# Kernel tuning notes

Hardware: AMD Instinct MI355X
Metric: run time of the kernel (lower is better)

## Reference

```python
import jax, jax.numpy as jnp
import numpy as np

B, L, A, HD, H = 4096, 512, 64, 1024, 32
EPS = 1e-5


def _ln(x, g, b):
    m = jnp.mean(x, axis=-1, keepdims=True)
    v = jnp.mean((x - m) ** 2, axis=-1, keepdims=True)
    return (x - m) * jax.lax.rsqrt(v + EPS) * g + b


def setup_inputs() -> dict:
    key = jax.random.key(0)
    ks = jax.random.split(key, 12)
    s = 0.02
    return {
        "z_0": jax.random.normal(ks[0], (B, L), jnp.float32),
        "actions": jax.random.normal(ks[1], (B, H, A), jnp.float32),
        "W1": jax.random.normal(ks[2], (L + A, HD), jnp.float32) * s,
        "b1": jnp.zeros((HD,), jnp.float32),
        "g1": jnp.ones((HD,), jnp.float32),
        "be1": jnp.zeros((HD,), jnp.float32),
        "W2": jax.random.normal(ks[3], (HD, HD), jnp.float32) * s,
        "b2": jnp.zeros((HD,), jnp.float32),
        "g2": jnp.ones((HD,), jnp.float32),
        "be2": jnp.zeros((HD,), jnp.float32),
        "W3": jax.random.normal(ks[4], (HD, L), jnp.float32) * s,
        "b3": jnp.zeros((L,), jnp.float32),
        "uW1": jax.random.normal(ks[5], (L, HD // 2), jnp.float32) * s,
        "ub1": jnp.zeros((HD // 2,), jnp.float32),
        "uW2": jax.random.normal(ks[6], (HD // 2, 1), jnp.float32) * s,
        "ub2": jnp.zeros((1,), jnp.float32),
        "gate": jnp.asarray(0.5, jnp.float32),
    }


def reference(z_0, actions, W1, b1, g1, be1, W2, b2, g2, be2, W3, b3,
              uW1, ub1, uW2, ub2, gate):
    gate_s = jax.nn.sigmoid(gate)

    def step_fn(z, a):
        za = jnp.concatenate([z, a], axis=-1)              # [B, L+A]
        h = jax.nn.gelu(_ln(za @ W1 + b1, g1, be1), approximate=False)
        h = jax.nn.gelu(_ln(h @ W2 + b2, g2, be2), approximate=False)
        dz = h @ W3 + b3                                   # [B, L]
        z_next = z + gate_s * dz
        u = jax.nn.gelu(z_next @ uW1 + ub1, approximate=False)
        sigma = jax.nn.softplus(u @ uW2 + ub2)             # [B, 1]
        return z_next, (z_next, sigma)

    a_seq = jnp.swapaxes(actions, 0, 1)                    # [H, B, A]
    _, (traj, sigs) = jax.lax.scan(step_fn, z_0, a_seq)
    return jnp.swapaxes(traj, 0, 1), jnp.swapaxes(sigs, 0, 1)
```

## Files before the change

kernel.cpp:

```cpp
#include <hip/hip_runtime.h>
#include <hip/hip_bf16.h>
#include <math.h>

#define B_SZ 4096
#define L_SZ 512
#define A_SZ 64
#define HD_SZ 1024
#define H_SZ 32

typedef __attribute__((ext_vector_type(8))) short bf16x8;
typedef __attribute__((ext_vector_type(4))) short s16x4;
typedef __attribute__((ext_vector_type(4))) float f32x4;

#define GLDS16(gsrc, ldst) __builtin_amdgcn_global_load_lds(              \
    (const __attribute__((address_space(1))) void*)(gsrc),                \
    (__attribute__((address_space(3))) void*)(ldst), 16, 0, 0)

template <int N> __device__ __forceinline__ void vmwait() {
  asm volatile("s_waitcnt vmcnt(%0)" :: "n"(N) : "memory");
}

__device__ __forceinline__ float gelu_exact(float x) {
  return 0.5f * x * (1.0f + erff(x * 0.70710678118654752f));
}

template <int BM, int BN, int MODE>
__global__ __launch_bounds__(256, 2) void gemm_kernel(
    const __hip_bfloat16* __restrict__ A0, int a0s,
    const __hip_bfloat16* __restrict__ A1, int a1s, int ksplit,
    const __hip_bfloat16* __restrict__ Bt,
    const float* __restrict__ bias,
    int N, int K,
    float* __restrict__ outf,
    float* __restrict__ z_cur,
    __hip_bfloat16* __restrict__ znb,
    float* __restrict__ traj,
    const float* __restrict__ gate,
    int t,
    float* __restrict__ zu,
    const float* __restrict__ ub1v,
    const float* __restrict__ uW2,
    float* __restrict__ sig_acc,
    __hip_bfloat16* __restrict__ outb) {
  constexpr int BK = 64;
  constexpr int ROWB = BK * 2;
  constexpr int FM = BM / 32, FN = BN / 32;
  constexpr int ABYTES = BM * ROWB;
  constexpr int BUFB = (BM + BN) * ROWB;
  constexpr int LOADS = (BM + BN) / 32;
  __shared__ __align__(16) char lds[3 * BUFB];

  const int tid = threadIdx.x;
  const int m0 = blockIdx.x * BM, n0 = blockIdx.y * BN;
  const int wave = tid >> 6, lane = tid & 63;
  const int l15 = lane & 15, lg = lane >> 4;
  const int wm = wave >> 1, wn = wave & 1;
  const int NK = K / BK;

  f32x4 acc[FM][FN];
#pragma unroll
  for (int mi = 0; mi < FM; ++mi)
#pragma unroll
    for (int ni = 0; ni < FN; ++ni) acc[mi][ni] = (f32x4){0.f, 0.f, 0.f, 0.f};

  auto stage = [&](int slot, int kt) {
    char* dst = lds + slot * BUFB;
    const int k0 = kt * BK;
    const __hip_bfloat16* Aptr;
    int As, kloc;
    if (k0 < ksplit) { Aptr = A0; As = a0s; kloc = k0; }
    else             { Aptr = A1; As = a1s; kloc = k0 - ksplit; }
#pragma unroll
    for (int i = 0; i < BM / 32; ++i) {
      int off = tid * 16 + i * 4096;
      int r = off >> 7;
      int csw = (off & 127) ^ ((r & 7) << 4);
      GLDS16(Aptr + (size_t)(m0 + r) * As + kloc + (csw >> 1), dst + off);
    }
#pragma unroll
    for (int i = 0; i < BN / 32; ++i) {
      int off = tid * 16 + i * 4096;
      int r = off >> 7;
      int csw = (off & 127) ^ ((r & 7) << 4);
      GLDS16(Bt + (size_t)(n0 + r) * K + k0 + (csw >> 1), dst + ABYTES + off);
    }
  };

  const int xrow = (l15 & 7) << 4;
  const int offs0 = (lg * 16) ^ xrow;
  const int aoff = (wm * (FM * 16) + l15) * ROWB;
  const int boff = ABYTES + (wn * (FN * 16) + l15) * ROWB;

  stage(0, 0);
  stage(1, 1);

  int buf = 0;
  for (int kt = 0; kt < NK; ++kt) {
    if (kt + 2 < NK) {
      int s2 = buf + 2; if (s2 >= 3) s2 -= 3;
      stage(s2, kt + 2);
      vmwait<2 * LOADS>();
    } else if (kt + 1 < NK) {
      vmwait<LOADS>();
    } else {
      vmwait<0>();
    }
    __builtin_amdgcn_s_barrier();
    asm volatile("" ::: "memory");

    const char* lb = lds + buf * BUFB;
    bf16x8 a_[FM][2], b_[FN][2];
#pragma unroll
    for (int mi = 0; mi < FM; ++mi) {
      a_[mi][0] = *(const bf16x8*)(lb + aoff + mi * (16 * ROWB) + offs0);
      a_[mi][1] = *(const bf16x8*)(lb + aoff + mi * (16 * ROWB) + (offs0 ^ 64));
    }
#pragma unroll
    for (int ni = 0; ni < FN; ++ni) {
      b_[ni][0] = *(const bf16x8*)(lb + boff + ni * (16 * ROWB) + offs0);
      b_[ni][1] = *(const bf16x8*)(lb + boff + ni * (16 * ROWB) + (offs0 ^ 64));
    }
#pragma unroll
    for (int s = 0; s < 2; ++s)
#pragma unroll
      for (int mi = 0; mi < FM; ++mi)
#pragma unroll
        for (int ni = 0; ni < FN; ++ni)
          acc[mi][ni] = __builtin_amdgcn_mfma_f32_16x16x32_bf16(
              a_[mi][s], b_[ni][s], acc[mi][ni], 0, 0, 0);

    asm volatile("" ::: "memory");
    __builtin_amdgcn_s_barrier();
    buf = (buf + 1 == 3) ? 0 : buf + 1;
  }

  if constexpr (MODE == 0 || MODE == 5) {
#pragma unroll
    for (int mi = 0; mi < FM; ++mi) {
#pragma unroll
      for (int ni = 0; ni < FN; ++ni) {
        int gcol = n0 + wn * (FN * 16) + ni * 16 + l15;
        float bv = bias[gcol];
#pragma unroll
        for (int r = 0; r < 4; ++r) {
          int grow = m0 + wm * (FM * 16) + mi * 16 + lg * 4 + r;
          float v = acc[mi][ni][r] + bv;
          if constexpr (MODE == 0)
            outb[(size_t)grow * N + gcol] = __float2bfloat16(v);
          else
            outf[(size_t)grow * N + gcol] = v;
        }
      }
    }
  } else {
    const float gs = 1.f / (1.f + expf(-gate[0]));
    if (n0 < L_SZ) {
#pragma unroll
      for (int mi = 0; mi < FM; ++mi) {
#pragma unroll
        for (int ni = 0; ni < FN; ++ni) {
          int gcol = n0 + wn * (FN * 16) + ni * 16 + l15;
          float bv = bias[gcol];
#pragma unroll
          for (int r = 0; r < 4; ++r) {
            int grow = m0 + wm * (FM * 16) + mi * 16 + lg * 4 + r;
            size_t zi = (size_t)grow * L_SZ + gcol;
            float zn = z_cur[zi] + gs * (acc[mi][ni][r] + bv);
            z_cur[zi] = zn;
            znb[zi] = __float2bfloat16(zn);
            traj[(size_t)grow * (H_SZ * L_SZ) + (size_t)t * L_SZ + gcol] = zn;
          }
        }
      }
    } else {
#pragma unroll
      for (int mi = 0; mi < FM; ++mi) {
        float p[4] = {0.f, 0.f, 0.f, 0.f};
#pragma unroll
        for (int ni = 0; ni < FN; ++ni) {
          int gcol = n0 + wn * (FN * 16) + ni * 16 + l15;
          int j = gcol - L_SZ;
          float bv = bias[gcol];
          float ub = ub1v[j];
          float w2 = uW2[j];
#pragma unroll
          for (int r = 0; r < 4; ++r) {
            int grow = m0 + wm * (FM * 16) + mi * 16 + lg * 4 + r;
            size_t ui = (size_t)grow * L_SZ + j;
            float zun = zu[ui] + gs * (acc[mi][ni][r] + bv);
            zu[ui] = zun;
            p[r] += gelu_exact(zun + ub) * w2;
          }
        }
#pragma unroll
        for (int o = 1; o < 16; o <<= 1) {
#pragma unroll
          for (int r = 0; r < 4; ++r) p[r] += __shfl_xor(p[r], o);
        }
        if (l15 == 0) {
          int rowb = m0 + wm * (FM * 16) + mi * 16 + lg * 4;
#pragma unroll
          for (int r = 0; r < 4; ++r)
            atomicAdd(&sig_acc[(size_t)(rowb + r) * H_SZ + t], p[r]);
        }
      }
    }
  }
}

__global__ __launch_bounds__(256) void ln_gelu_kernel(
    const __hip_bfloat16* __restrict__ x, const float* __restrict__ gam,
    const float* __restrict__ bet, __hip_bfloat16* __restrict__ out) {
  constexpr int N = HD_SZ;
  const int row = blockIdx.x;
  const int tid = threadIdx.x, lane = tid & 63, wave = tid >> 6;
  union { s16x4 sv; __hip_bfloat16 h[4]; } in;
  in.sv = *(const s16x4*)(x + (size_t)row * N + tid * 4);
  float v[4];
#pragma unroll
  for (int j = 0; j < 4; ++j) v[j] = __bfloat162float(in.h[j]);
  float s = v[0] + v[1] + v[2] + v[3];
  float s2 = v[0] * v[0] + v[1] * v[1] + v[2] * v[2] + v[3] * v[3];
#pragma unroll
  for (int o = 32; o; o >>= 1) {
    s += __shfl_xor(s, o);
    s2 += __shfl_xor(s2, o);
  }
  __shared__ float as_[4], as2_[4];
  if (lane == 0) { as_[wave] = s; as2_[wave] = s2; }
  __syncthreads();
  s = as_[0] + as_[1] + as_[2] + as_[3];
  s2 = as2_[0] + as2_[1] + as2_[2] + as2_[3];
  float mean = s * (1.f / N);
  float var = s2 * (1.f / N) - mean * mean;
  float rstd = rsqrtf(var + 1e-5f);
  f32x4 g = *(const f32x4*)(gam + tid * 4);
  f32x4 b = *(const f32x4*)(bet + tid * 4);
  union { __hip_bfloat16 h[4]; s16x4 sv; } o;
#pragma unroll
  for (int j = 0; j < 4; ++j) {
    float y = (v[j] - mean) * rstd * g[j] + b[j];
    o.h[j] = __float2bfloat16(gelu_exact(y));
  }
  *(s16x4*)(out + (size_t)row * N + tid * 4) = o.sv;
}

__global__ void transpose_cvt(const float* __restrict__ in,
                              __hip_bfloat16* __restrict__ out, int K, int N) {
  __shared__ float tile[32][33];
  const int n0 = blockIdx.x * 32, k0 = blockIdx.y * 32;
  const int tx = threadIdx.x, ty = threadIdx.y;
#pragma unroll
  for (int i = 0; i < 32; i += 8)
    tile[ty + i][tx] = in[(size_t)(k0 + ty + i) * N + (n0 + tx)];
  __syncthreads();
#pragma unroll
  for (int i = 0; i < 32; i += 8)
    out[(size_t)(n0 + ty + i) * K + (k0 + tx)] = __float2bfloat16(tile[tx][ty + i]);
}

__global__ __launch_bounds__(256) void w34_kernel(
    const float* __restrict__ W3, const float* __restrict__ uW1,
    __hip_bfloat16* __restrict__ W3c) {
  __shared__ float tA[16][17];
  __shared__ float tB[16][17];
  const int k0 = blockIdx.x * 16, j0 = blockIdx.y * 16;
  const int tx = threadIdx.x & 15, ty = threadIdx.x >> 4;
  float acc = 0.f;
  for (int i0 = 0; i0 < L_SZ; i0 += 16) {
    tA[ty][tx] = W3[(size_t)(k0 + ty) * L_SZ + i0 + tx];
    tB[ty][tx] = uW1[(size_t)(i0 + ty) * (HD_SZ / 2) + j0 + tx];
    __syncthreads();
#pragma unroll
    for (int i = 0; i < 16; ++i) acc += tA[ty][i] * tB[i][tx];
    __syncthreads();
  }
  W3c[(size_t)(L_SZ + j0 + tx) * HD_SZ + k0 + ty] = __float2bfloat16(acc);
}

__global__ void bias3_kernel(const float* __restrict__ b3,
                             const float* __restrict__ uW1,
                             float* __restrict__ bias3c) {
  int j = blockIdx.x * 256 + threadIdx.x;
  if (j >= L_SZ) return;
  bias3c[j] = b3[j];
  float s = 0.f;
  for (int i = 0; i < L_SZ; ++i) s += b3[i] * uW1[(size_t)i * (HD_SZ / 2) + j];
  bias3c[L_SZ + j] = s;
}

__global__ void cvt_bf16_kernel(const float* __restrict__ in,
                                __hip_bfloat16* __restrict__ out, int n4) {
  int i = blockIdx.x * 256 + threadIdx.x;
  if (i >= n4) return;
  f32x4 v = ((const f32x4*)in)[i];
  union { __hip_bfloat16 h[4]; s16x4 sv; } o;
#pragma unroll
  for (int j = 0; j < 4; ++j) o.h[j] = __float2bfloat16(v[j]);
  ((s16x4*)out)[i] = o.sv;
}

__global__ void init_z_kernel(const float* __restrict__ z0,
                              float* __restrict__ z_cur,
                              __hip_bfloat16* __restrict__ znb, int n4) {
  int i = blockIdx.x * 256 + threadIdx.x;
  if (i >= n4) return;
  f32x4 v = ((const f32x4*)z0)[i];
  ((f32x4*)z_cur)[i] = v;
  union { __hip_bfloat16 h[4]; s16x4 sv; } o;
#pragma unroll
  for (int j = 0; j < 4; ++j) o.h[j] = __float2bfloat16(v[j]);
  ((s16x4*)znb)[i] = o.sv;
}

__global__ void zero_kernel(float* __restrict__ p, int n) {
  int i = blockIdx.x * 256 + threadIdx.x;
  if (i < n) p[i] = 0.f;
}

__global__ void softplus_kernel(const float* __restrict__ acc,
                                const float* __restrict__ ub2,
                                float* __restrict__ out, int n) {
  int i = blockIdx.x * 256 + threadIdx.x;
  if (i >= n) return;
  float v = acc[i] + ub2[0];
  out[i] = v > 20.f ? v : log1pf(expf(v));
}

extern "C" void kernel_launch(void* const* d_in, const int* in_sizes, int n_in,
                              void* d_out, int out_size, void* d_ws,
                              size_t ws_size, hipStream_t stream) {
  const float* z0      = (const float*)d_in[0];
  const float* actions = (const float*)d_in[1];
  const float* W1  = (const float*)d_in[2];
  const float* b1  = (const float*)d_in[3];
  const float* g1  = (const float*)d_in[4];
  const float* be1 = (const float*)d_in[5];
  const float* W2  = (const float*)d_in[6];
  const float* b2  = (const float*)d_in[7];
  const float* g2  = (const float*)d_in[8];
  const float* be2 = (const float*)d_in[9];
  const float* W3  = (const float*)d_in[10];
  const float* b3  = (const float*)d_in[11];
  const float* uW1 = (const float*)d_in[12];
  const float* ub1 = (const float*)d_in[13];
  const float* uW2 = (const float*)d_in[14];
  const float* ub2 = (const float*)d_in[15];
  const float* gate = (const float*)d_in[16];

  char* w = (char*)d_ws;
  __hip_bfloat16* W1t = (__hip_bfloat16*)w;  w += (size_t)(L_SZ + A_SZ) * HD_SZ * 2;
  __hip_bfloat16* W2t = (__hip_bfloat16*)w;  w += (size_t)HD_SZ * HD_SZ * 2;
  __hip_bfloat16* W3c = (__hip_bfloat16*)w;  w += (size_t)HD_SZ * HD_SZ * 2;
  __hip_bfloat16* uW1t = (__hip_bfloat16*)w; w += (size_t)L_SZ * (HD_SZ / 2) * 2;
  __hip_bfloat16* actb = (__hip_bfloat16*)w; w += (size_t)B_SZ * H_SZ * A_SZ * 2;
  float* z_cur = (float*)w;                  w += (size_t)B_SZ * L_SZ * 4;
  __hip_bfloat16* znb = (__hip_bfloat16*)w;  w += (size_t)B_SZ * L_SZ * 2;
  float* zu = (float*)w;                     w += (size_t)B_SZ * L_SZ * 4;
  __hip_bfloat16* tws = (__hip_bfloat16*)w;  w += (size_t)B_SZ * HD_SZ * 2;
  __hip_bfloat16* hb = (__hip_bfloat16*)w;   w += (size_t)B_SZ * HD_SZ * 2;
  float* sig_acc = (float*)w;                w += (size_t)B_SZ * H_SZ * 4;
  float* bias3c = (float*)w;                 w += (size_t)HD_SZ * 4;
  float* zbias = (float*)w;                  w += (size_t)L_SZ * 4;

  float* trajOut = (float*)d_out;
  float* sigsOut = (float*)d_out + (size_t)B_SZ * H_SZ * L_SZ;

  dim3 tb(32, 8);
  transpose_cvt<<<dim3(HD_SZ / 32, (L_SZ + A_SZ) / 32), tb, 0, stream>>>(W1, W1t, L_SZ + A_SZ, HD_SZ);
  transpose_cvt<<<dim3(HD_SZ / 32, HD_SZ / 32), tb, 0, stream>>>(W2, W2t, HD_SZ, HD_SZ);
  transpose_cvt<<<dim3(L_SZ / 32, HD_SZ / 32), tb, 0, stream>>>(W3, W3c, HD_SZ, L_SZ);
  transpose_cvt<<<dim3((HD_SZ / 2) / 32, L_SZ / 32), tb, 0, stream>>>(uW1, uW1t, L_SZ, HD_SZ / 2);
  w34_kernel<<<dim3(HD_SZ / 16, L_SZ / 16), 256, 0, stream>>>(W3, uW1, W3c);
  bias3_kernel<<<2, 256, 0, stream>>>(b3, uW1, bias3c);

  cvt_bf16_kernel<<<(B_SZ * H_SZ * A_SZ / 4 + 255) / 256, 256, 0, stream>>>(
      actions, actb, B_SZ * H_SZ * A_SZ / 4);
  init_z_kernel<<<(B_SZ * L_SZ / 4 + 255) / 256, 256, 0, stream>>>(
      z0, z_cur, znb, B_SZ * L_SZ / 4);
  zero_kernel<<<(B_SZ * H_SZ + 255) / 256, 256, 0, stream>>>(sig_acc, B_SZ * H_SZ);
  zero_kernel<<<(L_SZ + 255) / 256, 256, 0, stream>>>(zbias, L_SZ);

  const int KSPLIT_NONE = 1 << 30;

  gemm_kernel<64, 128, 5><<<dim3(B_SZ / 64, L_SZ / 128), 256, 0, stream>>>(
      znb, L_SZ, nullptr, 0, KSPLIT_NONE, uW1t, zbias,
      L_SZ, L_SZ, zu, nullptr, nullptr, nullptr, nullptr, 0,
      nullptr, nullptr, nullptr, nullptr, nullptr);

  for (int t = 0; t < H_SZ; ++t) {
    gemm_kernel<64, 128, 0><<<dim3(B_SZ / 64, HD_SZ / 128), 256, 0, stream>>>(
        znb, L_SZ, actb + (size_t)t * A_SZ, H_SZ * A_SZ, L_SZ, W1t, b1,
        HD_SZ, L_SZ + A_SZ, nullptr, nullptr, nullptr, nullptr, nullptr, 0,
        nullptr, nullptr, nullptr, nullptr, tws);
    ln_gelu_kernel<<<B_SZ, 256, 0, stream>>>(tws, g1, be1, hb);
    gemm_kernel<64, 128, 0><<<dim3(B_SZ / 64, HD_SZ / 128), 256, 0, stream>>>(
        hb, HD_SZ, nullptr, 0, KSPLIT_NONE, W2t, b2,
        HD_SZ, HD_SZ, nullptr, nullptr, nullptr, nullptr, nullptr, 0,
        nullptr, nullptr, nullptr, nullptr, tws);
    ln_gelu_kernel<<<B_SZ, 256, 0, stream>>>(tws, g2, be2, hb);
    gemm_kernel<64, 128, 4><<<dim3(B_SZ / 64, HD_SZ / 128), 256, 0, stream>>>(
        hb, HD_SZ, nullptr, 0, KSPLIT_NONE, W3c, bias3c,
        HD_SZ, HD_SZ, nullptr, z_cur, znb, trajOut, gate, t,
        zu, ub1, uW2, sig_acc, nullptr);
  }
  softplus_kernel<<<(B_SZ * H_SZ + 255) / 256, 256, 0, stream>>>(
      sig_acc, ub2, sigsOut, B_SZ * H_SZ);
}
```

Measured before the change: 2.253 ms.

## Enlarge GEMM tiles to 128x128 and switch to double-buffered LDS pipeline

```diff
diff --git a/kernel.cpp b/kernel.cpp
--- a/kernel.cpp
+++ b/kernel.cpp
@@ -44,11 +44,12 @@
     __hip_bfloat16* __restrict__ outb) {
   constexpr int BK = 64;
   constexpr int ROWB = BK * 2;
-  constexpr int FM = BM / 32, FN = BN / 32;
+  constexpr int FM = BM / 64, FN = BN / 64;
+  constexpr int NFM = 2 * FM, NFN = 2 * FN;
   constexpr int ABYTES = BM * ROWB;
   constexpr int BUFB = (BM + BN) * ROWB;
   constexpr int LOADS = (BM + BN) / 32;
-  __shared__ __align__(16) char lds[3 * BUFB];
+  __shared__ __align__(16) char lds[2 * BUFB];
 
   const int tid = threadIdx.x;
   const int m0 = blockIdx.x * BM, n0 = blockIdx.y * BN;
@@ -57,11 +58,11 @@
   const int wm = wave >> 1, wn = wave & 1;
   const int NK = K / BK;
 
-  f32x4 acc[FM][FN];
-#pragma unroll
-  for (int mi = 0; mi < FM; ++mi)
-#pragma unroll
-    for (int ni = 0; ni < FN; ++ni) acc[mi][ni] = (f32x4){0.f, 0.f, 0.f, 0.f};
+  f32x4 acc[NFM][NFN];
+#pragma unroll
+  for (int mi = 0; mi < NFM; ++mi)
+#pragma unroll
+    for (int ni = 0; ni < NFN; ++ni) acc[mi][ni] = (f32x4){0.f, 0.f, 0.f, 0.f};
 
   auto stage = [&](int slot, int kt) {
     char* dst = lds + slot * BUFB;
@@ -88,19 +89,15 @@
 
   const int xrow = (l15 & 7) << 4;
   const int offs0 = (lg * 16) ^ xrow;
-  const int aoff = (wm * (FM * 16) + l15) * ROWB;
-  const int boff = ABYTES + (wn * (FN * 16) + l15) * ROWB;
+  const int aoff = (wm * (NFM * 16) + l15) * ROWB;
+  const int boff = ABYTES + (wn * (NFN * 16) + l15) * ROWB;
 
   stage(0, 0);
-  stage(1, 1);
 
   int buf = 0;
   for (int kt = 0; kt < NK; ++kt) {
-    if (kt + 2 < NK) {
-      int s2 = buf + 2; if (s2 >= 3) s2 -= 3;
-      stage(s2, kt + 2);
-      vmwait<2 * LOADS>();
-    } else if (kt + 1 < NK) {
+    if (kt + 1 < NK) {
+      stage(buf ^ 1, kt + 1);
       vmwait<LOADS>();
     } else {
       vmwait<0>();
@@ -109,41 +106,41 @@
     asm volatile("" ::: "memory");
 
     const char* lb = lds + buf * BUFB;
-    bf16x8 a_[FM][2], b_[FN][2];
-#pragma unroll
-    for (int mi = 0; mi < FM; ++mi) {
+    bf16x8 a_[NFM][2], b_[NFN][2];
+#pragma unroll
+    for (int mi = 0; mi < NFM; ++mi) {
       a_[mi][0] = *(const bf16x8*)(lb + aoff + mi * (16 * ROWB) + offs0);
       a_[mi][1] = *(const bf16x8*)(lb + aoff + mi * (16 * ROWB) + (offs0 ^ 64));
     }
 #pragma unroll
-    for (int ni = 0; ni < FN; ++ni) {
+    for (int ni = 0; ni < NFN; ++ni) {
       b_[ni][0] = *(const bf16x8*)(lb + boff + ni * (16 * ROWB) + offs0);
       b_[ni][1] = *(const bf16x8*)(lb + boff + ni * (16 * ROWB) + (offs0 ^ 64));
     }
 #pragma unroll
     for (int s = 0; s < 2; ++s)
 #pragma unroll
-      for (int mi = 0; mi < FM; ++mi)
-#pragma unroll
-        for (int ni = 0; ni < FN; ++ni)
+      for (int mi = 0; mi < NFM; ++mi)
+#pragma unroll
+        for (int ni = 0; ni < NFN; ++ni)
           acc[mi][ni] = __builtin_amdgcn_mfma_f32_16x16x32_bf16(
               a_[mi][s], b_[ni][s], acc[mi][ni], 0, 0, 0);
 
     asm volatile("" ::: "memory");
     __builtin_amdgcn_s_barrier();
-    buf = (buf + 1 == 3) ? 0 : buf + 1;
+    buf ^= 1;
   }
 
   if constexpr (MODE == 0 || MODE == 5) {
 #pragma unroll
-    for (int mi = 0; mi < FM; ++mi) {
-#pragma unroll
-      for (int ni = 0; ni < FN; ++ni) {
-        int gcol = n0 + wn * (FN * 16) + ni * 16 + l15;
+    for (int mi = 0; mi < NFM; ++mi) {
+#pragma unroll
+      for (int ni = 0; ni < NFN; ++ni) {
+        int gcol = n0 + wn * (NFN * 16) + ni * 16 + l15;
         float bv = bias[gcol];
 #pragma unroll
         for (int r = 0; r < 4; ++r) {
-          int grow = m0 + wm * (FM * 16) + mi * 16 + lg * 4 + r;
+          int grow = m0 + wm * (NFM * 16) + mi * 16 + lg * 4 + r;
           float v = acc[mi][ni][r] + bv;
           if constexpr (MODE == 0)
             outb[(size_t)grow * N + gcol] = __float2bfloat16(v);
@@ -156,14 +153,14 @@
     const float gs = 1.f / (1.f + expf(-gate[0]));
     if (n0 < L_SZ) {
 #pragma unroll
-      for (int mi = 0; mi < FM; ++mi) {
-#pragma unroll
-        for (int ni = 0; ni < FN; ++ni) {
-          int gcol = n0 + wn * (FN * 16) + ni * 16 + l15;
+      for (int mi = 0; mi < NFM; ++mi) {
+#pragma unroll
+        for (int ni = 0; ni < NFN; ++ni) {
+          int gcol = n0 + wn * (NFN * 16) + ni * 16 + l15;
           float bv = bias[gcol];
 #pragma unroll
           for (int r = 0; r < 4; ++r) {
-            int grow = m0 + wm * (FM * 16) + mi * 16 + lg * 4 + r;
+            int grow = m0 + wm * (NFM * 16) + mi * 16 + lg * 4 + r;
             size_t zi = (size_t)grow * L_SZ + gcol;
             float zn = z_cur[zi] + gs * (acc[mi][ni][r] + bv);
             z_cur[zi] = zn;
@@ -174,18 +171,18 @@
       }
     } else {
 #pragma unroll
-      for (int mi = 0; mi < FM; ++mi) {
+      for (int mi = 0; mi < NFM; ++mi) {
         float p[4] = {0.f, 0.f, 0.f, 0.f};
 #pragma unroll
-        for (int ni = 0; ni < FN; ++ni) {
-          int gcol = n0 + wn * (FN * 16) + ni * 16 + l15;
+        for (int ni = 0; ni < NFN; ++ni) {
+          int gcol = n0 + wn * (NFN * 16) + ni * 16 + l15;
           int j = gcol - L_SZ;
           float bv = bias[gcol];
           float ub = ub1v[j];
           float w2 = uW2[j];
 #pragma unroll
           for (int r = 0; r < 4; ++r) {
-            int grow = m0 + wm * (FM * 16) + mi * 16 + lg * 4 + r;
+            int grow = m0 + wm * (NFM * 16) + mi * 16 + lg * 4 + r;
             size_t ui = (size_t)grow * L_SZ + j;
             float zun = zu[ui] + gs * (acc[mi][ni][r] + bv);
             zu[ui] = zun;
@@ -198,7 +195,7 @@
           for (int r = 0; r < 4; ++r) p[r] += __shfl_xor(p[r], o);
         }
         if (l15 == 0) {
-          int rowb = m0 + wm * (FM * 16) + mi * 16 + lg * 4;
+          int rowb = m0 + wm * (NFM * 16) + mi * 16 + lg * 4;
 #pragma unroll
           for (int r = 0; r < 4; ++r)
             atomicAdd(&sig_acc[(size_t)(rowb + r) * H_SZ + t], p[r]);
@@ -383,23 +380,23 @@
 
   const int KSPLIT_NONE = 1 << 30;
 
-  gemm_kernel<64, 128, 5><<<dim3(B_SZ / 64, L_SZ / 128), 256, 0, stream>>>(
+  gemm_kernel<128, 128, 5><<<dim3(B_SZ / 128, L_SZ / 128), 256, 0, stream>>>(
       znb, L_SZ, nullptr, 0, KSPLIT_NONE, uW1t, zbias,
       L_SZ, L_SZ, zu, nullptr, nullptr, nullptr, nullptr, 0,
       nullptr, nullptr, nullptr, nullptr, nullptr);
 
   for (int t = 0; t < H_SZ; ++t) {
-    gemm_kernel<64, 128, 0><<<dim3(B_SZ / 64, HD_SZ / 128), 256, 0, stream>>>(
+    gemm_kernel<128, 128, 0><<<dim3(B_SZ / 128, HD_SZ / 128), 256, 0, stream>>>(
         znb, L_SZ, actb + (size_t)t * A_SZ, H_SZ * A_SZ, L_SZ, W1t, b1,
         HD_SZ, L_SZ + A_SZ, nullptr, nullptr, nullptr, nullptr, nullptr, 0,
         nullptr, nullptr, nullptr, nullptr, tws);
     ln_gelu_kernel<<<B_SZ, 256, 0, stream>>>(tws, g1, be1, hb);
-    gemm_kernel<64, 128, 0><<<dim3(B_SZ / 64, HD_SZ / 128), 256, 0, stream>>>(
+    gemm_kernel<128, 128, 0><<<dim3(B_SZ / 128, HD_SZ / 128), 256, 0, stream>>>(
         hb, HD_SZ, nullptr, 0, KSPLIT_NONE, W2t, b2,
         HD_SZ, HD_SZ, nullptr, nullptr, nullptr, nullptr, nullptr, 0,
         nullptr, nullptr, nullptr, nullptr, tws);
     ln_gelu_kernel<<<B_SZ, 256, 0, stream>>>(tws, g2, be2, hb);
-    gemm_kernel<64, 128, 4><<<dim3(B_SZ / 64, HD_SZ / 128), 256, 0, stream>>>(
+    gemm_kernel<128, 128, 4><<<dim3(B_SZ / 128, HD_SZ / 128), 256, 0, stream>>>(
         hb, HD_SZ, nullptr, 0, KSPLIT_NONE, W3c, bias3c,
         HD_SZ, HD_SZ, nullptr, z_cur, znb, trajOut, gate, t,
         zu, ub1, uW2, sig_acc, nullptr);
```

Measured after the change: 2.570 ms. 1.14x slower.

## Remap GEMM blocks for per-XCD L2 locality and use wave-per-row LayerNorm

Applied to the files above, without the earlier changes.

```diff
diff --git a/kernel.cpp b/kernel.cpp
--- a/kernel.cpp
+++ b/kernel.cpp
@@ -30,7 +30,7 @@
     const __hip_bfloat16* __restrict__ A1, int a1s, int ksplit,
     const __hip_bfloat16* __restrict__ Bt,
     const float* __restrict__ bias,
-    int N, int K,
+    int N, int K, int NT,
     float* __restrict__ outf,
     float* __restrict__ z_cur,
     __hip_bfloat16* __restrict__ znb,
@@ -51,7 +51,9 @@
   __shared__ __align__(16) char lds[3 * BUFB];
 
   const int tid = threadIdx.x;
-  const int m0 = blockIdx.x * BM, n0 = blockIdx.y * BN;
+  const int q = gridDim.x >> 3;
+  const int g = (blockIdx.x & 7) * q + (blockIdx.x >> 3);
+  const int m0 = (g / NT) * BM, n0 = (g % NT) * BN;
   const int wave = tid >> 6, lane = tid & 63;
   const int l15 = lane & 15, lg = lane >> 4;
   const int wm = wave >> 1, wn = wave & 1;
@@ -212,37 +214,44 @@
     const __hip_bfloat16* __restrict__ x, const float* __restrict__ gam,
     const float* __restrict__ bet, __hip_bfloat16* __restrict__ out) {
   constexpr int N = HD_SZ;
-  const int row = blockIdx.x;
-  const int tid = threadIdx.x, lane = tid & 63, wave = tid >> 6;
-  union { s16x4 sv; __hip_bfloat16 h[4]; } in;
-  in.sv = *(const s16x4*)(x + (size_t)row * N + tid * 4);
-  float v[4];
-#pragma unroll
-  for (int j = 0; j < 4; ++j) v[j] = __bfloat162float(in.h[j]);
-  float s = v[0] + v[1] + v[2] + v[3];
-  float s2 = v[0] * v[0] + v[1] * v[1] + v[2] * v[2] + v[3] * v[3];
+  const int row = blockIdx.x * 4 + (threadIdx.x >> 6);
+  const int lane = threadIdx.x & 63;
+  const __hip_bfloat16* xr = x + (size_t)row * N + lane * 16;
+  union { bf16x8 v; __hip_bfloat16 h[8]; } i0, i1;
+  i0.v = *(const bf16x8*)xr;
+  i1.v = *(const bf16x8*)(xr + 8);
+  float v[16];
+#pragma unroll
+  for (int j = 0; j < 8; ++j) v[j] = __bfloat162float(i0.h[j]);
+#pragma unroll
+  for (int j = 0; j < 8; ++j) v[8 + j] = __bfloat162float(i1.h[j]);
+  float s = 0.f, s2 = 0.f;
+#pragma unroll
+  for (int j = 0; j < 16; ++j) { s += v[j]; s2 += v[j] * v[j]; }
 #pragma unroll
   for (int o = 32; o; o >>= 1) {
     s += __shfl_xor(s, o);
     s2 += __shfl_xor(s2, o);
   }
-  __shared__ float as_[4], as2_[4];
-  if (lane == 0) { as_[wave] = s; as2_[wave] = s2; }
-  __syncthreads();
-  s = as_[0] + as_[1] + as_[2] + as_[3];
-  s2 = as2_[0] + as2_[1] + as2_[2] + as2_[3];
   float mean = s * (1.f / N);
   float var = s2 * (1.f / N) - mean * mean;
   float rstd = rsqrtf(var + 1e-5f);
-  f32x4 g = *(const f32x4*)(gam + tid * 4);
-  f32x4 b = *(const f32x4*)(bet + tid * 4);
-  union { __hip_bfloat16 h[4]; s16x4 sv; } o;
-#pragma unroll
-  for (int j = 0; j < 4; ++j) {
-    float y = (v[j] - mean) * rstd * g[j] + b[j];
-    o.h[j] = __float2bfloat16(gelu_exact(y));
-  }
-  *(s16x4*)(out + (size_t)row * N + tid * 4) = o.sv;
+  const float* gp = gam + lane * 16;
+  const float* bp = bet + lane * 16;
+  union { __hip_bfloat16 h[8]; bf16x8 v; } o0, o1;
+#pragma unroll
+  for (int j = 0; j < 8; ++j) {
+    float y = (v[j] - mean) * rstd * gp[j] + bp[j];
+    o0.h[j] = __float2bfloat16(gelu_exact(y));
+  }
+#pragma unroll
+  for (int j = 0; j < 8; ++j) {
+    float y = (v[8 + j] - mean) * rstd * gp[8 + j] + bp[8 + j];
+    o1.h[j] = __float2bfloat16(gelu_exact(y));
+  }
+  __hip_bfloat16* op = out + (size_t)row * N + lane * 16;
+  *(bf16x8*)op = o0.v;
+  *(bf16x8*)(op + 8) = o1.v;
 }
 
 __global__ void transpose_cvt(const float* __restrict__ in,
@@ -383,25 +392,25 @@
 
   const int KSPLIT_NONE = 1 << 30;
 
-  gemm_kernel<64, 128, 5><<<dim3(B_SZ / 64, L_SZ / 128), 256, 0, stream>>>(
+  gemm_kernel<64, 128, 5><<<(B_SZ / 64) * (L_SZ / 128), 256, 0, stream>>>(
       znb, L_SZ, nullptr, 0, KSPLIT_NONE, uW1t, zbias,
-      L_SZ, L_SZ, zu, nullptr, nullptr, nullptr, nullptr, 0,
+      L_SZ, L_SZ, L_SZ / 128, zu, nullptr, nullptr, nullptr, nullptr, 0,
       nullptr, nullptr, nullptr, nullptr, nullptr);
 
   for (int t = 0; t < H_SZ; ++t) {
-    gemm_kernel<64, 128, 0><<<dim3(B_SZ / 64, HD_SZ / 128), 256, 0, stream>>>(
+    gemm_kernel<64, 128, 0><<<(B_SZ / 64) * (HD_SZ / 128), 256, 0, stream>>>(
         znb, L_SZ, actb + (size_t)t * A_SZ, H_SZ * A_SZ, L_SZ, W1t, b1,
-        HD_SZ, L_SZ + A_SZ, nullptr, nullptr, nullptr, nullptr, nullptr, 0,
-        nullptr, nullptr, nullptr, nullptr, tws);
-    ln_gelu_kernel<<<B_SZ, 256, 0, stream>>>(tws, g1, be1, hb);
-    gemm_kernel<64, 128, 0><<<dim3(B_SZ / 64, HD_SZ / 128), 256, 0, stream>>>(
+        HD_SZ, L_SZ + A_SZ, HD_SZ / 128, nullptr, nullptr, nullptr, nullptr,
+        nullptr, 0, nullptr, nullptr, nullptr, nullptr, tws);
+    ln_gelu_kernel<<<B_SZ / 4, 256, 0, stream>>>(tws, g1, be1, hb);
+    gemm_kernel<64, 128, 0><<<(B_SZ / 64) * (HD_SZ / 128), 256, 0, stream>>>(
         hb, HD_SZ, nullptr, 0, KSPLIT_NONE, W2t, b2,
-        HD_SZ, HD_SZ, nullptr, nullptr, nullptr, nullptr, nullptr, 0,
-        nullptr, nullptr, nullptr, nullptr, tws);
-    ln_gelu_kernel<<<B_SZ, 256, 0, stream>>>(tws, g2, be2, hb);
-    gemm_kernel<64, 128, 4><<<dim3(B_SZ / 64, HD_SZ / 128), 256, 0, stream>>>(
+        HD_SZ, HD_SZ, HD_SZ / 128, nullptr, nullptr, nullptr, nullptr,
+        nullptr, 0, nullptr, nullptr, nullptr, nullptr, tws);
+    ln_gelu_kernel<<<B_SZ / 4, 256, 0, stream>>>(tws, g2, be2, hb);
+    gemm_kernel<64, 128, 4><<<(B_SZ / 64) * (HD_SZ / 128), 256, 0, stream>>>(
         hb, HD_SZ, nullptr, 0, KSPLIT_NONE, W3c, bias3c,
-        HD_SZ, HD_SZ, nullptr, z_cur, znb, trajOut, gate, t,
+        HD_SZ, HD_SZ, HD_SZ / 128, nullptr, z_cur, znb, trajOut, gate, t,
         zu, ub1, uW2, sig_acc, nullptr);
   }
   softplus_kernel<<<(B_SZ * H_SZ + 255) / 256, 256, 0, stream>>>(
```

After: 3.062 ms. +35.9%, slower.

## Fuse LayerNorm+GELU into GEMM epilogue via cross-block row-stat atomics and spin barrier

Applied to the files above, without the earlier changes.

```diff
diff --git a/kernel.cpp b/kernel.cpp
--- a/kernel.cpp
+++ b/kernel.cpp
@@ -41,7 +41,12 @@
     const float* __restrict__ ub1v,
     const float* __restrict__ uW2,
     float* __restrict__ sig_acc,
-    __hip_bfloat16* __restrict__ outb) {
+    __hip_bfloat16* __restrict__ outb,
+    const float* __restrict__ gamv,
+    const float* __restrict__ betv,
+    float* __restrict__ rowsum,
+    float* __restrict__ rowsq,
+    int* __restrict__ cnt) {
   constexpr int BK = 64;
   constexpr int ROWB = BK * 2;
   constexpr int FM = BM / 32, FN = BN / 32;
@@ -134,7 +139,7 @@
     buf = (buf + 1 == 3) ? 0 : buf + 1;
   }
 
-  if constexpr (MODE == 0 || MODE == 5) {
+  if constexpr (MODE == 5) {
 #pragma unroll
     for (int mi = 0; mi < FM; ++mi) {
 #pragma unroll
@@ -144,11 +149,82 @@
 #pragma unroll
         for (int r = 0; r < 4; ++r) {
           int grow = m0 + wm * (FM * 16) + mi * 16 + lg * 4 + r;
-          float v = acc[mi][ni][r] + bv;
-          if constexpr (MODE == 0)
-            outb[(size_t)grow * N + gcol] = __float2bfloat16(v);
-          else
-            outf[(size_t)grow * N + gcol] = v;
+          outf[(size_t)grow * N + gcol] = acc[mi][ni][r] + bv;
+        }
+      }
+    }
+  } else if constexpr (MODE == 6) {
+    float bv[FN];
+#pragma unroll
+    for (int ni = 0; ni < FN; ++ni)
+      bv[ni] = bias[n0 + wn * (FN * 16) + ni * 16 + l15];
+#pragma unroll
+    for (int mi = 0; mi < FM; ++mi) {
+      float s_[4], q_[4];
+#pragma unroll
+      for (int r = 0; r < 4; ++r) {
+        float s = 0.f, q = 0.f;
+#pragma unroll
+        for (int ni = 0; ni < FN; ++ni) {
+          float v = acc[mi][ni][r] + bv[ni];
+          s += v; q += v * v;
+        }
+        s_[r] = s; q_[r] = q;
+      }
+#pragma unroll
+      for (int o = 1; o < 16; o <<= 1) {
+#pragma unroll
+        for (int r = 0; r < 4; ++r) {
+          s_[r] += __shfl_xor(s_[r], o);
+          q_[r] += __shfl_xor(q_[r], o);
+        }
+      }
+      if (l15 == 0) {
+        int rowb = m0 + wm * (FM * 16) + mi * 16 + lg * 4;
+#pragma unroll
+        for (int r = 0; r < 4; ++r) {
+          atomicAdd(&rowsum[rowb + r], s_[r]);
+          atomicAdd(&rowsq[rowb + r], q_[r]);
+        }
+      }
+    }
+    __threadfence();
+    __syncthreads();
+    if (tid == 0) {
+      __hip_atomic_fetch_add(&cnt[blockIdx.x], 1, __ATOMIC_ACQ_REL,
+                             __HIP_MEMORY_SCOPE_AGENT);
+      while (__hip_atomic_load(&cnt[blockIdx.x], __ATOMIC_ACQUIRE,
+                               __HIP_MEMORY_SCOPE_AGENT) < (N / BN)) {
+        __builtin_amdgcn_s_sleep(8);
+      }
+    }
+    __syncthreads();
+    const float invN = 1.f / (float)N;
+#pragma unroll
+    for (int mi = 0; mi < FM; ++mi) {
+      int rowb = m0 + wm * (FM * 16) + mi * 16 + lg * 4;
+      float mean_[4], rstd_[4];
+#pragma unroll
+      for (int r = 0; r < 4; ++r) {
+        float sm = __hip_atomic_load(&rowsum[rowb + r], __ATOMIC_RELAXED,
+                                     __HIP_MEMORY_SCOPE_AGENT);
+        float sq = __hip_atomic_load(&rowsq[rowb + r], __ATOMIC_RELAXED,
+                                     __HIP_MEMORY_SCOPE_AGENT);
+        float mn = sm * invN;
+        float vr = sq * invN - mn * mn;
+        mean_[r] = mn;
+        rstd_[r] = rsqrtf(vr + 1e-5f);
+      }
+#pragma unroll
+      for (int ni = 0; ni < FN; ++ni) {
+        int gcol = n0 + wn * (FN * 16) + ni * 16 + l15;
+        float gm = gamv[gcol], be = betv[gcol];
+#pragma unroll
+        for (int r = 0; r < 4; ++r) {
+          float v = acc[mi][ni][r] + bv[ni];
+          float y = (v - mean_[r]) * rstd_[r] * gm + be;
+          outb[(size_t)(rowb + r) * N + gcol] =
+              __float2bfloat16(gelu_exact(y));
         }
       }
     }
@@ -206,43 +282,6 @@
       }
     }
   }
-}
-
-__global__ __launch_bounds__(256) void ln_gelu_kernel(
-    const __hip_bfloat16* __restrict__ x, const float* __restrict__ gam,
-    const float* __restrict__ bet, __hip_bfloat16* __restrict__ out) {
-  constexpr int N = HD_SZ;
-  const int row = blockIdx.x;
-  const int tid = threadIdx.x, lane = tid & 63, wave = tid >> 6;
-  union { s16x4 sv; __hip_bfloat16 h[4]; } in;
-  in.sv = *(const s16x4*)(x + (size_t)row * N + tid * 4);
-  float v[4];
-#pragma unroll
-  for (int j = 0; j < 4; ++j) v[j] = __bfloat162float(in.h[j]);
-  float s = v[0] + v[1] + v[2] + v[3];
-  float s2 = v[0] * v[0] + v[1] * v[1] + v[2] * v[2] + v[3] * v[3];
-#pragma unroll
-  for (int o = 32; o; o >>= 1) {
-    s += __shfl_xor(s, o);
-    s2 += __shfl_xor(s2, o);
-  }
-  __shared__ float as_[4], as2_[4];
-  if (lane == 0) { as_[wave] = s; as2_[wave] = s2; }
-  __syncthreads();
-  s = as_[0] + as_[1] + as_[2] + as_[3];
-  s2 = as2_[0] + as2_[1] + as2_[2] + as2_[3];
-  float mean = s * (1.f / N);
-  float var = s2 * (1.f / N) - mean * mean;
-  float rstd = rsqrtf(var + 1e-5f);
-  f32x4 g = *(const f32x4*)(gam + tid * 4);
-  f32x4 b = *(const f32x4*)(bet + tid * 4);
-  union { __hip_bfloat16 h[4]; s16x4 sv; } o;
-#pragma unroll
-  for (int j = 0; j < 4; ++j) {
-    float y = (v[j] - mean) * rstd * g[j] + b[j];
-    o.h[j] = __float2bfloat16(gelu_exact(y));
-  }
-  *(s16x4*)(out + (size_t)row * N + tid * 4) = o.sv;
 }
 
 __global__ void transpose_cvt(const float* __restrict__ in,
@@ -357,11 +396,16 @@
   float* z_cur = (float*)w;                  w += (size_t)B_SZ * L_SZ * 4;
   __hip_bfloat16* znb = (__hip_bfloat16*)w;  w += (size_t)B_SZ * L_SZ * 2;
   float* zu = (float*)w;                     w += (size_t)B_SZ * L_SZ * 4;
-  __hip_bfloat16* tws = (__hip_bfloat16*)w;  w += (size_t)B_SZ * HD_SZ * 2;
-  __hip_bfloat16* hb = (__hip_bfloat16*)w;   w += (size_t)B_SZ * HD_SZ * 2;
+  __hip_bfloat16* h1b = (__hip_bfloat16*)w;  w += (size_t)B_SZ * HD_SZ * 2;
+  __hip_bfloat16* h2b = (__hip_bfloat16*)w;  w += (size_t)B_SZ * HD_SZ * 2;
+  float* bias3c = (float*)w;                 w += (size_t)HD_SZ * 4;
+  float* zero_base = (float*)w;
   float* sig_acc = (float*)w;                w += (size_t)B_SZ * H_SZ * 4;
-  float* bias3c = (float*)w;                 w += (size_t)HD_SZ * 4;
   float* zbias = (float*)w;                  w += (size_t)L_SZ * 4;
+  float* rowsum = (float*)w;                 w += (size_t)64 * B_SZ * 4;
+  float* rowsq = (float*)w;                  w += (size_t)64 * B_SZ * 4;
+  int* cnt = (int*)w;                        w += (size_t)64 * 64 * 4;
+  const int ZERO_N = B_SZ * H_SZ + L_SZ + 64 * B_SZ + 64 * B_SZ + 64 * 64;
 
   float* trajOut = (float*)d_out;
   float* sigsOut = (float*)d_out + (size_t)B_SZ * H_SZ * L_SZ;
@@ -378,31 +422,35 @@
       actions, actb, B_SZ * H_SZ * A_SZ / 4);
   init_z_kernel<<<(B_SZ * L_SZ / 4 + 255) / 256, 256, 0, stream>>>(
       z0, z_cur, znb, B_SZ * L_SZ / 4);
-  zero_kernel<<<(B_SZ * H_SZ + 255) / 256, 256, 0, stream>>>(sig_acc, B_SZ * H_SZ);
-  zero_kernel<<<(L_SZ + 255) / 256, 256, 0, stream>>>(zbias, L_SZ);
+  zero_kernel<<<(ZERO_N + 255) / 256, 256, 0, stream>>>(zero_base, ZERO_N);
 
   const int KSPLIT_NONE = 1 << 30;
 
   gemm_kernel<64, 128, 5><<<dim3(B_SZ / 64, L_SZ / 128), 256, 0, stream>>>(
       znb, L_SZ, nullptr, 0, KSPLIT_NONE, uW1t, zbias,
       L_SZ, L_SZ, zu, nullptr, nullptr, nullptr, nullptr, 0,
+      nullptr, nullptr, nullptr, nullptr, nullptr,
       nullptr, nullptr, nullptr, nullptr, nullptr);
 
   for (int t = 0; t < H_SZ; ++t) {
-    gemm_kernel<64, 128, 0><<<dim3(B_SZ / 64, HD_SZ / 128), 256, 0, stream>>>(
+    const int use1 = t * 2, use2 = t * 2 + 1;
+    gemm_kernel<64, 128, 6><<<dim3(B_SZ / 64, HD_SZ / 128), 256, 0, stream>>>(
         znb, L_SZ, actb + (size_t)t * A_SZ, H_SZ * A_SZ, L_SZ, W1t, b1,
         HD_SZ, L_SZ + A_SZ, nullptr, nullptr, nullptr, nullptr, nullptr, 0,
-        nullptr, nullptr, nullptr, nullptr, tws);
-    ln_gelu_kernel<<<B_SZ, 256, 0, stream>>>(tws, g1, be1, hb);
-    gemm_kernel<64, 128, 0><<<dim3(B_SZ / 64, HD_SZ / 128), 256, 0, stream>>>(
-        hb, HD_SZ, nullptr, 0, KSPLIT_NONE, W2t, b2,
+        nullptr, nullptr, nullptr, nullptr, h1b,
+        g1, be1, rowsum + (size_t)use1 * B_SZ, rowsq + (size_t)use1 * B_SZ,
+        cnt + use1 * 64);
+    gemm_kernel<64, 128, 6><<<dim3(B_SZ / 64, HD_SZ / 128), 256, 0, stream>>>(
+        h1b, HD_SZ, nullptr, 0, KSPLIT_NONE, W2t, b2,
         HD_SZ, HD_SZ, nullptr, nullptr, nullptr, nullptr, nullptr, 0,
-        nullptr, nullptr, nullptr, nullptr, tws);
-    ln_gelu_kernel<<<B_SZ, 256, 0, stream>>>(tws, g2, be2, hb);
+        nullptr, nullptr, nullptr, nullptr, h2b,
+        g2, be2, rowsum + (size_t)use2 * B_SZ, rowsq + (size_t)use2 * B_SZ,
+        cnt + use2 * 64);
     gemm_kernel<64, 128, 4><<<dim3(B_SZ / 64, HD_SZ / 128), 256, 0, stream>>>(
-        hb, HD_SZ, nullptr, 0, KSPLIT_NONE, W3c, bias3c,
+        h2b, HD_SZ, nullptr, 0, KSPLIT_NONE, W3c, bias3c,
         HD_SZ, HD_SZ, nullptr, z_cur, znb, trajOut, gate, t,
-        zu, ub1, uW2, sig_acc, nullptr);
+        zu, ub1, uW2, sig_acc, nullptr,
+        nullptr, nullptr, nullptr, nullptr, nullptr);
   }
   softplus_kernel<<<(B_SZ * H_SZ + 255) / 256, 256, 0, stream>>>(
       sig_acc, ub2, sigsOut, B_SZ * H_SZ);
```

Measured after the change: 4.937 ms. 2.19x slower.
